# Performance work log

Hardware: AMD Instinct MI355X
Metric: run time of the kernel (lower is better)

The kernel has to match this reference:

```python
import jax, jax.numpy as jnp
import numpy as np

EMBED = 1024
HEADS = 16
HEAD_DIM = EMBED // HEADS


def setup_inputs() -> dict:
    key = jax.random.key(0)
    ks = jax.random.split(key, 8)
    N, L = 2, 2048
    s = 0.02
    return {
        "values": jax.random.normal(ks[0], (N, L, EMBED), jnp.float32),
        "keys": jax.random.normal(ks[1], (N, L, EMBED), jnp.float32),
        "queries": jax.random.normal(ks[2], (N, L, EMBED), jnp.float32),
        # per-head projection weights, SHARED across heads (nn.Linear(head_dim, head_dim))
        "Wv": jax.random.normal(ks[3], (HEAD_DIM, HEAD_DIM), jnp.float32) * s,
        "Wk": jax.random.normal(ks[4], (HEAD_DIM, HEAD_DIM), jnp.float32) * s,
        "Wq": jax.random.normal(ks[5], (HEAD_DIM, HEAD_DIM), jnp.float32) * s,
        "Wo": jax.random.normal(ks[6], (EMBED, EMBED), jnp.float32) * s,
        "bo": jax.random.normal(ks[7], (EMBED,), jnp.float32) * s,
    }


def reference(values, keys, queries, Wv, Wk, Wq, Wo, bo):
    N, Lq, _ = queries.shape
    Lk = keys.shape[1]
    Lv = values.shape[1]
    # split heads: (N, L, H, D)
    v = values.reshape(N, Lv, HEADS, HEAD_DIM)
    k = keys.reshape(N, Lk, HEADS, HEAD_DIM)
    q = queries.reshape(N, Lq, HEADS, HEAD_DIM)
    # per-head linear (weight shared across heads); nn.Linear computes x @ W.T
    v = jnp.einsum('nlhd,ed->nlhe', v, Wv)
    k = jnp.einsum('nlhd,ed->nlhe', k, Wk)
    q = jnp.einsum('nlhd,ed->nlhe', q, Wq)
    # scores (N, H, Lq, Lk); NOTE: scale uses sqrt(embed_size), as in the original
    scores = jnp.einsum('nqhd,nkhd->nhqk', q, k) / jnp.sqrt(jnp.float32(EMBED))
    attn = jax.nn.softmax(scores, axis=-1)
    out = jnp.einsum('nhql,nlhd->nqhd', attn, v).reshape(N, Lq, EMBED)
    out = out @ Wo.T + bo
    return out
```

## Files before the change

### kernel.cpp

```cpp
#include <hip/hip_runtime.h>
#include <hip/hip_bf16.h>

#define EMBED 1024
#define HEADS 16
#define HD 64
#define NB 2
#define LSEQ 2048

typedef __bf16 bf16x8 __attribute__((ext_vector_type(8)));
typedef float f32x4 __attribute__((ext_vector_type(4)));

static __device__ __forceinline__ __bf16 f2b(float x) {
    union { __hip_bfloat16 h; __bf16 b; } u;
    u.h = __float2bfloat16(x);
    return u.b;
}
static __device__ __forceinline__ bf16x8 cvt8(float4 a, float4 b) {
    bf16x8 r;
    r[0] = f2b(a.x); r[1] = f2b(a.y); r[2] = f2b(a.z); r[3] = f2b(a.w);
    r[4] = f2b(b.x); r[5] = f2b(b.y); r[6] = f2b(b.z); r[7] = f2b(b.w);
    return r;
}
static __device__ __forceinline__ unsigned short b2u(float x) {
    union { __hip_bfloat16 h; unsigned short u; } c;
    c.h = __float2bfloat16(x);
    return c.u;
}

#define GLD16(g, l) __builtin_amdgcn_global_load_lds( \
    (const __attribute__((address_space(1))) void*)(g), \
    (__attribute__((address_space(3))) void*)(l), 16, 0, 0)


__global__ __launch_bounds__(256) void proj_kernel(
    const float* __restrict__ vals,
    const float* __restrict__ keys,
    const float* __restrict__ quer,
    const float* __restrict__ Wv,
    const float* __restrict__ Wk,
    const float* __restrict__ Wq,
    __hip_bfloat16* __restrict__ QF,
    __hip_bfloat16* __restrict__ KF,
    __hip_bfloat16* __restrict__ VF)
{
    int b      = blockIdx.x;
    int tensor = b % 3;
    int rem    = b / 3;
    int n      = rem >> 9;
    int lt     = (rem >> 4) & 31;
    int h      = rem & 15;
    int t = threadIdx.x, w = t >> 6, lane = t & 63;
    int m16 = lane & 15, quad = lane >> 4;
    int l0 = lt * 64 + w * 16;

    const float* X = (tensor == 0) ? quer : (tensor == 1 ? keys : vals);
    const float* W = (tensor == 0) ? Wq   : (tensor == 1 ? Wk   : Wv);
    float scale = (tensor == 0) ? (1.44269504088896340736f / 32.0f) : 1.0f;

    const float* xb = X + ((size_t)n * LSEQ + l0 + m16) * EMBED + h * HD + quad * 8;
    bf16x8 xf[2];
#pragma unroll
    for (int kk = 0; kk < 2; ++kk)
        xf[kk] = cvt8(*(const float4*)(xb + kk * 32), *(const float4*)(xb + kk * 32 + 4));

    bf16x8 wf[4][2];
#pragma unroll
    for (int f = 0; f < 4; ++f)
#pragma unroll
        for (int kk = 0; kk < 2; ++kk) {
            const float* wp = W + (f * 16 + m16) * HD + kk * 32 + quad * 8;
            wf[f][kk] = cvt8(*(const float4*)wp, *(const float4*)(wp + 4));
        }

    size_t nhb = (size_t)(n * HEADS + h) * 131072;
    if (tensor != 2) {
        f32x4 acc[4] = {};
#pragma unroll
        for (int f = 0; f < 4; ++f) {
            acc[f] = __builtin_amdgcn_mfma_f32_16x16x32_bf16(wf[f][0], xf[0], acc[f], 0, 0, 0);
            acc[f] = __builtin_amdgcn_mfma_f32_16x16x32_bf16(wf[f][1], xf[1], acc[f], 0, 0, 0);
        }
        int key = l0 + m16;
#pragma unroll
        for (int f = 0; f < 4; ++f) {
            union { ushort4 u; unsigned short s[4]; } p;
#pragma unroll
            for (int r = 0; r < 4; ++r) p.s[r] = b2u(acc[f][r] * scale);
            int kk   = f >> 1;
            int qk2  = (f & 1) * 2 + (quad >> 1);
            int j4   = (quad & 1) * 4;
            __hip_bfloat16* dst;
            if (tensor == 0) {
                dst = QF + nhb + (size_t)(l0 >> 4) * 1024 + kk * 512
                    + (qk2 * 16 + m16) * 8 + j4;
            } else {
                dst = KF + nhb + (size_t)(key >> 5) * 2048
                    + ((key & 1) * 2 + kk) * 512
                    + (qk2 * 16 + ((key & 31) >> 1)) * 8 + j4;
            }
            *(ushort4*)dst = p.u;
        }
    } else {
        f32x4 acc[4] = {};
#pragma unroll
        for (int f = 0; f < 4; ++f) {
            acc[f] = __builtin_amdgcn_mfma_f32_16x16x32_bf16(xf[0], wf[f][0], acc[f], 0, 0, 0);
            acc[f] = __builtin_amdgcn_mfma_f32_16x16x32_bf16(xf[1], wf[f][1], acc[f], 0, 0, 0);
        }
        int keyq  = l0 + quad * 4;
        int c     = keyq >> 5;
        int quadv = (keyq & 31) >> 3;
        int j4    = (quad & 1) * 4;
#pragma unroll
        for (int f = 0; f < 4; ++f) {
            union { ushort4 u; unsigned short s[4]; } p;
#pragma unroll
            for (int r = 0; r < 4; ++r) p.s[r] = b2u(acc[f][r]);
            __hip_bfloat16* dst = VF + nhb + (size_t)c * 2048 + f * 512
                + quadv * 128 + m16 * 8 + j4;
            *(ushort4*)dst = p.u;
        }
    }
}

__global__ __launch_bounds__(256) void wcvt_kernel(
    const float* __restrict__ Wo, __hip_bfloat16* __restrict__ Wob)
{
    int base = (blockIdx.x * 256 + threadIdx.x) * 16;
#pragma unroll
    for (int j = 0; j < 16; j += 4) {
        float4 w4 = *(const float4*)(Wo + base + j);
        __hip_bfloat16 o[4] = {
            __float2bfloat16(w4.x), __float2bfloat16(w4.y),
            __float2bfloat16(w4.z), __float2bfloat16(w4.w)};
        *(ushort4*)(Wob + base + j) = *(const ushort4*)o;
    }
}

#define CHUNKS 32

#define LOADK(KFR, c_) do { \
    const __hip_bfloat16* kc_ = kp + (size_t)(c_) * 2048; \
    KFR[0][0] = *(const bf16x8*)(kc_); \
    KFR[0][1] = *(const bf16x8*)(kc_ + 512); \
    KFR[1][0] = *(const bf16x8*)(kc_ + 1024); \
    KFR[1][1] = *(const bf16x8*)(kc_ + 1536); \
} while (0)

#define LOADV(c_) do { \
    const __hip_bfloat16* vc_ = vp + (size_t)(c_) * 2048; \
    vf[0] = *(const bf16x8*)(vc_); \
    vf[1] = *(const bf16x8*)(vc_ + 512); \
    vf[2] = *(const bf16x8*)(vc_ + 1024); \
    vf[3] = *(const bf16x8*)(vc_ + 1536); \
} while (0)

#define SCORE(KFR, BUF) do { \
    f32x4 s_[2][2]; \
    __builtin_amdgcn_s_setprio(1); \
    _Pragma("unroll") \
    for (int tq_ = 0; tq_ < 2; ++tq_) { \
        _Pragma("unroll") \
        for (int t2_ = 0; t2_ < 2; ++t2_) { \
            f32x4 z_ = {}; \
            z_ = __builtin_amdgcn_mfma_f32_16x16x32_bf16(qf[tq_][0], KFR[t2_][0], z_, 0, 0, 0); \
            z_ = __builtin_amdgcn_mfma_f32_16x16x32_bf16(qf[tq_][1], KFR[t2_][1], z_, 0, 0, 0); \
            s_[tq_][t2_] = z_; \
        } \
    } \
    __builtin_amdgcn_s_setprio(0); \
    _Pragma("unroll") \
    for (int tq_ = 0; tq_ < 2; ++tq_) { \
        _Pragma("unroll") \
        for (int r_ = 0; r_ < 4; ++r_) { \
            float e0_ = __builtin_amdgcn_exp2f(s_[tq_][0][r_]); \
            float e1_ = __builtin_amdgcn_exp2f(s_[tq_][1][r_]); \
            unsigned u_ = __builtin_amdgcn_perm( \
                __float_as_uint(e1_), __float_as_uint(e0_), 0x07060302); \
            *(unsigned*)&Pb[BUF][w][tq_ * 16 + quad * 4 + r_][2 * m16] = u_; \
        } \
    } \
} while (0)

#define PVSTEP(BUF) do { \
    bf16x8 pf0_ = *(const bf16x8*)&Pb[BUF][w][m16][quad * 8]; \
    bf16x8 pf1_ = *(const bf16x8*)&Pb[BUF][w][16 + m16][quad * 8]; \
    __builtin_amdgcn_s_setprio(1); \
    _Pragma("unroll") \
    for (int f_ = 0; f_ < 4; ++f_) { \
        of[0][f_] = __builtin_amdgcn_mfma_f32_16x16x32_bf16(pf0_, vf[f_], of[0][f_], 0, 0, 0); \
        of[1][f_] = __builtin_amdgcn_mfma_f32_16x16x32_bf16(pf1_, vf[f_], of[1][f_], 0, 0, 0); \
    } \
    lsa[0] = __builtin_amdgcn_mfma_f32_16x16x32_bf16(pf0_, onesf, lsa[0], 0, 0, 0); \
    lsa[1] = __builtin_amdgcn_mfma_f32_16x16x32_bf16(pf1_, onesf, lsa[1], 0, 0, 0); \
    __builtin_amdgcn_s_setprio(0); \
} while (0)

__global__ __launch_bounds__(256) void attn_kernel(
    const __hip_bfloat16* __restrict__ QF,
    const __hip_bfloat16* __restrict__ KF,
    const __hip_bfloat16* __restrict__ VF,
    __hip_bfloat16* __restrict__ AO)
{
    __shared__ __align__(16) __hip_bfloat16 Pb[2][4][32][40];

    int i  = blockIdx.x;
    int x  = i & 7, r2 = i >> 3;
    int nh = x * 4 + (r2 >> 5);
    int qblk = r2 & 31;

    int t = threadIdx.x, w = t >> 6, lane = t & 63;
    int m16 = lane & 15, quad = lane >> 4;
    int qh = w & 1, kh = w >> 1;
    int q0 = qblk * 64 + qh * 32;
    size_t nhb = (size_t)nh * 131072;

    const __hip_bfloat16* qb = QF + nhb + (size_t)(q0 >> 4) * 1024 + lane * 8;
    bf16x8 qf[2][2];
#pragma unroll
    for (int tq = 0; tq < 2; ++tq)
#pragma unroll
        for (int kk = 0; kk < 2; ++kk)
            qf[tq][kk] = *(const bf16x8*)(qb + tq * 1024 + kk * 512);

    const __hip_bfloat16* kp = KF + nhb + (size_t)(kh * 32) * 2048 + lane * 8;
    const __hip_bfloat16* vp = VF + nhb + (size_t)(kh * 32) * 2048 + lane * 8;

    bf16x8 onesf;
#pragma unroll
    for (int j = 0; j < 8; ++j) onesf[j] = f2b(1.0f);

    f32x4 of[2][4] = {};
    f32x4 lsa[2] = {};
    bf16x8 kfa[2][2], kfb[2][2], vf[4];

    LOADK(kfa, 0);
    LOADK(kfb, 1);
    SCORE(kfa, 0);
    LOADV(0);

#pragma unroll 1
    for (int tt = 0; tt < 15; ++tt) {
        int c = 2 * tt;
        LOADK(kfa, c + 2);
        SCORE(kfb, 1);
        PVSTEP(0);
        LOADV(c + 1);
        LOADK(kfb, c + 3);
        SCORE(kfa, 0);
        PVSTEP(1);
        LOADV(c + 2);
    }
    SCORE(kfb, 1);
    PVSTEP(0);
    LOADV(31);
    PVSTEP(1);

    __syncthreads();
    float* Cb = (float*)&Pb[0][0][0][0];
    if (kh == 1) {
        int base = qh * 2560;
#pragma unroll
        for (int tq = 0; tq < 2; ++tq)
#pragma unroll
            for (int f = 0; f < 4; ++f)
                *(f32x4*)&Cb[base + (tq * 4 + f) * 256 + lane * 4] = of[tq][f];
#pragma unroll
        for (int tq = 0; tq < 2; ++tq)
#pragma unroll
            for (int r = 0; r < 4; ++r)
                Cb[base + 2048 + (tq * 4 + r) * 64 + lane] = lsa[tq][r];
    }
    __syncthreads();
    if (kh == 0) {
        int base = qh * 2560;
#pragma unroll
        for (int tq = 0; tq < 2; ++tq)
#pragma unroll
            for (int f = 0; f < 4; ++f)
                of[tq][f] += *(const f32x4*)&Cb[base + (tq * 4 + f) * 256 + lane * 4];
        int n = nh >> 4, h = nh & 15;
#pragma unroll
        for (int tq = 0; tq < 2; ++tq)
#pragma unroll
            for (int r = 0; r < 4; ++r) {
                float lt2 = lsa[tq][r] + Cb[base + 2048 + (tq * 4 + r) * 64 + lane];
                float rinv = 1.0f / lt2;
                int qrow = q0 + tq * 16 + quad * 4 + r;
#pragma unroll
                for (int f = 0; f < 4; ++f) {
                    int col = h * HD + f * 16 + m16;
                    AO[((size_t)n * LSEQ + qrow) * EMBED + col] =
                        __float2bfloat16(of[tq][f][r] * rinv);
                }
            }
    }
}

__global__ __launch_bounds__(256) void outproj_kernel(
    const __hip_bfloat16* __restrict__ AO,
    const __hip_bfloat16* __restrict__ Wob,
    const float* __restrict__ bo,
    float* __restrict__ out)
{
    __shared__ __align__(16) __hip_bfloat16 As[2][64][32];
    __shared__ __align__(16) __hip_bfloat16 Bs[2][64][32];

    int b  = blockIdx.x;
    int mt = b >> 4, nt = b & 15;
    int m0 = mt * 64, n0 = nt * 64;
    int t = threadIdx.x, w = t >> 6, lane = t & 63;
    int m16 = lane & 15, quad = lane >> 4;

    int srow = lane >> 2;
    int scol = (lane & 3) * 8;

    const __hip_bfloat16* Ab = AO  + (size_t)m0 * EMBED;
    const __hip_bfloat16* Bb = Wob + (size_t)n0 * EMBED;

    f32x4 acc[4] = {};
    for (int k0 = 0; k0 < EMBED; k0 += 64) {
        __syncthreads();
        GLD16(Ab + (size_t)(w * 16 + srow) * EMBED + k0 +      scol, &As[0][w * 16][0]);
        GLD16(Ab + (size_t)(w * 16 + srow) * EMBED + k0 + 32 + scol, &As[1][w * 16][0]);
        GLD16(Bb + (size_t)(w * 16 + srow) * EMBED + k0 +      scol, &Bs[0][w * 16][0]);
        GLD16(Bb + (size_t)(w * 16 + srow) * EMBED + k0 + 32 + scol, &Bs[1][w * 16][0]);
        __syncthreads();

        bf16x8 af[2], bfr[2][4];
#pragma unroll
        for (int kk = 0; kk < 2; ++kk)
            af[kk] = *(const bf16x8*)&As[kk][w * 16 + m16][quad * 8];
#pragma unroll
        for (int kk = 0; kk < 2; ++kk)
#pragma unroll
            for (int tb = 0; tb < 4; ++tb)
                bfr[kk][tb] = *(const bf16x8*)&Bs[kk][tb * 16 + m16][quad * 8];
#pragma unroll
        for (int tb = 0; tb < 4; ++tb) {
            acc[tb] = __builtin_amdgcn_mfma_f32_16x16x32_bf16(af[0], bfr[0][tb], acc[tb], 0, 0, 0);
            acc[tb] = __builtin_amdgcn_mfma_f32_16x16x32_bf16(af[1], bfr[1][tb], acc[tb], 0, 0, 0);
        }
    }

#pragma unroll
    for (int tb = 0; tb < 4; ++tb) {
        int col = n0 + tb * 16 + m16;
        float bias = bo[col];
#pragma unroll
        for (int r = 0; r < 4; ++r) {
            int row = m0 + w * 16 + quad * 4 + r;
            out[(size_t)row * EMBED + col] = acc[tb][r] + bias;
        }
    }
}

extern "C" void kernel_launch(void* const* d_in, const int* in_sizes, int n_in,
                              void* d_out, int out_size, void* d_ws, size_t ws_size,
                              hipStream_t stream) {
    const float* vals = (const float*)d_in[0];
    const float* keys = (const float*)d_in[1];
    const float* quer = (const float*)d_in[2];
    const float* Wv   = (const float*)d_in[3];
    const float* Wk   = (const float*)d_in[4];
    const float* Wq   = (const float*)d_in[5];
    const float* Wo   = (const float*)d_in[6];
    const float* bo   = (const float*)d_in[7];
    float* out = (float*)d_out;

    __hip_bfloat16* ws = (__hip_bfloat16*)d_ws;
    const size_t PE = (size_t)NB * HEADS * LSEQ * HD;
    __hip_bfloat16* QF  = ws;
    __hip_bfloat16* KF  = ws + PE;
    __hip_bfloat16* VF  = ws + 2 * PE;
    __hip_bfloat16* AO  = ws + 3 * PE;
    __hip_bfloat16* Wob = ws + 4 * PE;

    proj_kernel<<<3 * NB * (LSEQ / 64) * HEADS, 256, 0, stream>>>(
        vals, keys, quer, Wv, Wk, Wq, QF, KF, VF);
    wcvt_kernel<<<256, 256, 0, stream>>>(Wo, Wob);
    attn_kernel<<<1024, 256, 0, stream>>>(QF, KF, VF, AO);
    outproj_kernel<<<1024, 256, 0, stream>>>(AO, Wob, bo, out);
}
```

Measured before the change: 182.3 us.

## Fold Wo conversion into projection kernel and double-buffer out-projection GEMM

The separate Wo fp32-to-bf16 conversion kernel is merged into the projection kernel as 256 extra blocks, which removes one launch. The out-projection GEMM gets double-buffered LDS staging, so the next k-tile's async global-to-LDS loads overlap the current tile's MFMAs, with one barrier per iteration instead of two. Blocks are remapped so neighbouring block IDs cover different M tiles, spreading work across XCDs and L2. The attention kernel reuses a hoisted zero accumulator for its first score MFMA. The price is twice the LDS in the out-projection and a possible race if an async load into a buffer can still land while other waves are reading it.

```diff
diff --git a/kernel.cpp b/kernel.cpp
--- a/kernel.cpp
+++ b/kernel.cpp
@@ -39,10 +39,25 @@
     const float* __restrict__ Wv,
     const float* __restrict__ Wk,
     const float* __restrict__ Wq,
+    const float* __restrict__ Wo,
     __hip_bfloat16* __restrict__ QF,
     __hip_bfloat16* __restrict__ KF,
-    __hip_bfloat16* __restrict__ VF)
+    __hip_bfloat16* __restrict__ VF,
+    __hip_bfloat16* __restrict__ Wob)
 {
+    if (blockIdx.x >= 3072) {
+        int base = ((blockIdx.x - 3072) * 256 + threadIdx.x) * 16;
+#pragma unroll
+        for (int j = 0; j < 16; j += 4) {
+            float4 w4 = *(const float4*)(Wo + base + j);
+            __hip_bfloat16 o[4] = {
+                __float2bfloat16(w4.x), __float2bfloat16(w4.y),
+                __float2bfloat16(w4.z), __float2bfloat16(w4.w)};
+            *(ushort4*)(Wob + base + j) = *(const ushort4*)o;
+        }
+        return;
+    }
+
     int b      = blockIdx.x;
     int tensor = b % 3;
     int rem    = b / 3;
@@ -123,20 +138,6 @@
     }
 }
 
-__global__ __launch_bounds__(256) void wcvt_kernel(
-    const float* __restrict__ Wo, __hip_bfloat16* __restrict__ Wob)
-{
-    int base = (blockIdx.x * 256 + threadIdx.x) * 16;
-#pragma unroll
-    for (int j = 0; j < 16; j += 4) {
-        float4 w4 = *(const float4*)(Wo + base + j);
-        __hip_bfloat16 o[4] = {
-            __float2bfloat16(w4.x), __float2bfloat16(w4.y),
-            __float2bfloat16(w4.z), __float2bfloat16(w4.w)};
-        *(ushort4*)(Wob + base + j) = *(const ushort4*)o;
-    }
-}
-
 #define CHUNKS 32
 
 #define LOADK(KFR, c_) do { \
@@ -162,8 +163,8 @@
     for (int tq_ = 0; tq_ < 2; ++tq_) { \
         _Pragma("unroll") \
         for (int t2_ = 0; t2_ < 2; ++t2_) { \
-            f32x4 z_ = {}; \
-            z_ = __builtin_amdgcn_mfma_f32_16x16x32_bf16(qf[tq_][0], KFR[t2_][0], z_, 0, 0, 0); \
+            f32x4 z_; \
+            z_ = __builtin_amdgcn_mfma_f32_16x16x32_bf16(qf[tq_][0], KFR[t2_][0], zf, 0, 0, 0); \
             z_ = __builtin_amdgcn_mfma_f32_16x16x32_bf16(qf[tq_][1], KFR[t2_][1], z_, 0, 0, 0); \
             s_[tq_][t2_] = z_; \
         } \
@@ -229,6 +230,7 @@
     bf16x8 onesf;
 #pragma unroll
     for (int j = 0; j < 8; ++j) onesf[j] = f2b(1.0f);
+    const f32x4 zf = {};
 
     f32x4 of[2][4] = {};
     f32x4 lsa[2] = {};
@@ -303,11 +305,12 @@
     const float* __restrict__ bo,
     float* __restrict__ out)
 {
-    __shared__ __align__(16) __hip_bfloat16 As[2][64][32];
-    __shared__ __align__(16) __hip_bfloat16 Bs[2][64][32];
+    __shared__ __align__(16) __hip_bfloat16 As[2][2][64][32];
+    __shared__ __align__(16) __hip_bfloat16 Bs[2][2][64][32];
 
     int b  = blockIdx.x;
-    int mt = b >> 4, nt = b & 15;
+    int wk = (b & 7) * 128 + (b >> 3);
+    int mt = wk >> 4, nt = wk & 15;
     int m0 = mt * 64, n0 = nt * 64;
     int t = threadIdx.x, w = t >> 6, lane = t & 63;
     int m16 = lane & 15, quad = lane >> 4;
@@ -318,29 +321,36 @@
     const __hip_bfloat16* Ab = AO  + (size_t)m0 * EMBED;
     const __hip_bfloat16* Bb = Wob + (size_t)n0 * EMBED;
 
+#define STAGE_OP(bb, k0_) do { \
+    GLD16(Ab + (size_t)(w * 16 + srow) * EMBED + (k0_) +      scol, &As[bb][0][w * 16][0]); \
+    GLD16(Ab + (size_t)(w * 16 + srow) * EMBED + (k0_) + 32 + scol, &As[bb][1][w * 16][0]); \
+    GLD16(Bb + (size_t)(w * 16 + srow) * EMBED + (k0_) +      scol, &Bs[bb][0][w * 16][0]); \
+    GLD16(Bb + (size_t)(w * 16 + srow) * EMBED + (k0_) + 32 + scol, &Bs[bb][1][w * 16][0]); \
+} while (0)
+
     f32x4 acc[4] = {};
-    for (int k0 = 0; k0 < EMBED; k0 += 64) {
-        __syncthreads();
-        GLD16(Ab + (size_t)(w * 16 + srow) * EMBED + k0 +      scol, &As[0][w * 16][0]);
-        GLD16(Ab + (size_t)(w * 16 + srow) * EMBED + k0 + 32 + scol, &As[1][w * 16][0]);
-        GLD16(Bb + (size_t)(w * 16 + srow) * EMBED + k0 +      scol, &Bs[0][w * 16][0]);
-        GLD16(Bb + (size_t)(w * 16 + srow) * EMBED + k0 + 32 + scol, &Bs[1][w * 16][0]);
-        __syncthreads();
-
+    STAGE_OP(0, 0);
+    __syncthreads();
+
+#pragma unroll 2
+    for (int ks = 0; ks < 16; ++ks) {
+        if (ks < 15) STAGE_OP((ks + 1) & 1, (ks + 1) * 64);
+        int cur = ks & 1;
         bf16x8 af[2], bfr[2][4];
 #pragma unroll
         for (int kk = 0; kk < 2; ++kk)
-            af[kk] = *(const bf16x8*)&As[kk][w * 16 + m16][quad * 8];
+            af[kk] = *(const bf16x8*)&As[cur][kk][w * 16 + m16][quad * 8];
 #pragma unroll
         for (int kk = 0; kk < 2; ++kk)
 #pragma unroll
             for (int tb = 0; tb < 4; ++tb)
-                bfr[kk][tb] = *(const bf16x8*)&Bs[kk][tb * 16 + m16][quad * 8];
+                bfr[kk][tb] = *(const bf16x8*)&Bs[cur][kk][tb * 16 + m16][quad * 8];
 #pragma unroll
         for (int tb = 0; tb < 4; ++tb) {
             acc[tb] = __builtin_amdgcn_mfma_f32_16x16x32_bf16(af[0], bfr[0][tb], acc[tb], 0, 0, 0);
             acc[tb] = __builtin_amdgcn_mfma_f32_16x16x32_bf16(af[1], bfr[1][tb], acc[tb], 0, 0, 0);
         }
+        __syncthreads();
     }
 
 #pragma unroll
@@ -353,6 +363,7 @@
             out[(size_t)row * EMBED + col] = acc[tb][r] + bias;
         }
     }
+#undef STAGE_OP
 }
 
 extern "C" void kernel_launch(void* const* d_in, const int* in_sizes, int n_in,
@@ -376,9 +387,8 @@
     __hip_bfloat16* AO  = ws + 3 * PE;
     __hip_bfloat16* Wob = ws + 4 * PE;
 
-    proj_kernel<<<3 * NB * (LSEQ / 64) * HEADS, 256, 0, stream>>>(
-        vals, keys, quer, Wv, Wk, Wq, QF, KF, VF);
-    wcvt_kernel<<<256, 256, 0, stream>>>(Wo, Wob);
+    proj_kernel<<<3 * NB * (LSEQ / 64) * HEADS + 256, 256, 0, stream>>>(
+        vals, keys, quer, Wv, Wk, Wq, Wo, QF, KF, VF, Wob);
     attn_kernel<<<1024, 256, 0, stream>>>(QF, KF, VF, AO);
     outproj_kernel<<<1024, 256, 0, stream>>>(AO, Wob, bo, out);
 }
```

Measured after the change: 182.6 us. Within noise of the previous version (+0.2%).
